# Optimization experiments

Hardware: AMD Instinct MI355X
Metric: run time of the kernel (lower is better)

## Reference

```python
import jax, jax.numpy as jnp
import numpy as np

N = 50000        # nodes
E = 800_000      # edges (avg degree 16)
D_IN, D_HID, D_OUT = 512, 512, 256
P_DROP = 0.5


def setup_inputs() -> dict:
    key = jax.random.key(0)
    k0, k1, k2, k3 = jax.random.split(key, 4)
    x = jax.random.normal(k0, (N, D_IN), dtype=jnp.float32)
    edge_index = jax.random.randint(k1, (2, E), 0, N, dtype=jnp.int64)
    W1 = jax.random.normal(k2, (D_HID, D_IN), dtype=jnp.float32) * 0.02
    b1 = jnp.zeros((D_HID,), dtype=jnp.float32)
    W2 = jax.random.normal(k3, (D_OUT, D_HID), dtype=jnp.float32) * 0.02
    b2 = jnp.zeros((D_OUT,), dtype=jnp.float32)
    return {"x": x, "edge_index": edge_index, "W1": W1, "b1": b1, "W2": W2, "b2": b2}


def _gcn_norm(edge_index, n):
    # add self loops, then symmetric GCN normalization: D^-1/2 (A+I) D^-1/2
    src, dst = edge_index[0], edge_index[1]
    loops = jnp.arange(n, dtype=src.dtype)
    src = jnp.concatenate([src, loops])
    dst = jnp.concatenate([dst, loops])
    deg = jax.ops.segment_sum(jnp.ones_like(src, dtype=jnp.float32), dst, num_segments=n)
    dinv = jax.lax.rsqrt(deg)  # deg >= 1 because of self loops
    norm = dinv[src] * dinv[dst]  # [E+N]
    return src, dst, norm


def _propagate(x, src, dst, norm):
    # out[i] = sum_{(j->i)} norm_e * x[j]
    return jax.ops.segment_sum(x[src] * norm[:, None], dst, num_segments=x.shape[0])


def reference(x, edge_index, W1, b1, W2, b2):
    src, dst, norm = _gcn_norm(edge_index, x.shape[0])
    # SGConv layer 1 (K=1): propagate then linear
    h = _propagate(x, src, dst, norm) @ W1.T + b1
    h = jax.nn.relu(h)
    # F.dropout(p) with training=True default -> deterministic fixed-key mask here
    keep = jax.random.bernoulli(jax.random.key(42), 1.0 - P_DROP, h.shape)
    embedding = jnp.where(keep, h / (1.0 - P_DROP), 0.0)
    # SGConv layer 2
    out = _propagate(embedding, src, dst, norm) @ W2.T + b2
    return embedding, out
```

## Files before the change

kernel.cpp:

```cpp
#include <hip/hip_runtime.h>

typedef unsigned short u16t;
typedef __attribute__((ext_vector_type(8))) short short8;
typedef __attribute__((ext_vector_type(4))) short short4v;
typedef __attribute__((ext_vector_type(4))) float f32x4;
typedef __attribute__((ext_vector_type(4))) unsigned short u16x4;

__device__ __forceinline__ float bf2f(short b) {
  return __uint_as_float(((unsigned)(unsigned short)b) << 16);
}
__device__ __forceinline__ u16t f2bf(float f) {
  unsigned u = __float_as_uint(f);
  u += 0x7FFFu + ((u >> 16) & 1u);
  return (u16t)(u >> 16);
}

__device__ __forceinline__ bool keep_mask(unsigned flat) {
  const unsigned k0 = 0u, k1 = 42u;
  const unsigned k2 = k0 ^ k1 ^ 0x1BD11BDAu;
  unsigned x0 = 0u + k0;
  unsigned x1 = flat + k1;
#define TF_R(r) { x0 += x1; x1 = (x1 << r) | (x1 >> (32 - r)); x1 ^= x0; }
  TF_R(13) TF_R(15) TF_R(26) TF_R(6)  x0 += k1; x1 += k2 + 1u;
  TF_R(17) TF_R(29) TF_R(16) TF_R(24) x0 += k2; x1 += k0 + 2u;
  TF_R(13) TF_R(15) TF_R(26) TF_R(6)  x0 += k0; x1 += k1 + 3u;
  TF_R(17) TF_R(29) TF_R(16) TF_R(24) x0 += k1; x1 += k2 + 4u;
  TF_R(13) TF_R(15) TF_R(26) TF_R(6)  x0 += k2; x1 += k0 + 5u;
#undef TF_R
  return ((x0 ^ x1) >> 31) == 0u;
}

__device__ __forceinline__ void load_lds16(const u16t* g, u16t* l) {
  __builtin_amdgcn_global_load_lds((__attribute__((address_space(1))) void*)g,
                                   (__attribute__((address_space(3))) void*)l,
                                   16, 0, 0);
}

__global__ void cvt_bf16(const float* __restrict__ s, u16t* __restrict__ d, int n) {
  int i = (blockIdx.x * 256 + threadIdx.x) * 4;
  if (i < n) {
    f32x4 v = *(const f32x4*)&s[i];
    u16x4 o = { f2bf(v.x), f2bf(v.y), f2bf(v.z), f2bf(v.w) };
    *(u16x4*)&d[i] = o;
  }
}

__global__ __launch_bounds__(256) void cvt_x_mask(const float* __restrict__ s,
    u16t* __restrict__ d, unsigned* __restrict__ mask, int n, int nwords) {
  int t = blockIdx.x * 256 + threadIdx.x;
  int i = t * 4;
  if (i < n) {
    f32x4 v = *(const f32x4*)&s[i];
    u16x4 o = { f2bf(v.x), f2bf(v.y), f2bf(v.z), f2bf(v.w) };
    *(u16x4*)&d[i] = o;
  }
  if (t < nwords) {
    unsigned base = (unsigned)t * 32u;
    unsigned m = 0u;
    for (int k = 0; k < 32; ++k) m |= (keep_mask(base + (unsigned)k) ? 1u : 0u) << k;
    mask[t] = m;
  }
}

__global__ void count_edges(const int* __restrict__ dst, int E, int* __restrict__ cnt) {
  int e = blockIdx.x * 256 + threadIdx.x;
  if (e < E) atomicAdd(&cnt[dst[e]], 1);
}

__global__ __launch_bounds__(256) void rowp_build(const int* __restrict__ cnt,
    int* __restrict__ rowp, int* __restrict__ cursor, float* __restrict__ dinv,
    int* __restrict__ gctr, int n) {
  __shared__ int sd[256];
  __shared__ int sbase;
  const int tid = threadIdx.x;
  const int i = blockIdx.x * 256 + tid;
  int c = (i < n) ? cnt[i] : 0;
  int v = c;
  sd[tid] = v;
  __syncthreads();
  for (int o = 1; o < 256; o <<= 1) {
    int t = (tid >= o) ? sd[tid - o] : 0;
    __syncthreads();
    v += t;
    sd[tid] = v;
    __syncthreads();
  }
  if (tid == 255) sbase = atomicAdd(gctr, v);
  __syncthreads();
  if (i < n) {
    int start = sbase + v - c;
    rowp[i] = start;
    cursor[i] = start;
    dinv[i] = rsqrtf((float)(c + 1));
  }
}

__global__ void fill_csr(const int* __restrict__ src, const int* __restrict__ dst, int E,
                         int* __restrict__ cursor, u16t* __restrict__ col) {
  int e = blockIdx.x * 256 + threadIdx.x;
  if (e < E) {
    int d = dst[e];
    int pos = atomicAdd(&cursor[d], 1);
    col[pos] = (u16t)src[e];
  }
}

__global__ __launch_bounds__(256) void gemm_bt_sl(const u16t* __restrict__ A,
                                                  const u16t* __restrict__ B,
                                                  u16t* __restrict__ C,
                                                  int K, int Mrows,
                                                  const float* __restrict__ dinv,
                                                  int Nclamp) {
  __shared__ __align__(16) u16t lA[128 * 32];
  __shared__ __align__(16) u16t lB[128 * 32];
  const int tid = threadIdx.x;
  const int wave = tid >> 6, lane = tid & 63;
  const int wm = (wave & 1) * 64, wn = (wave >> 1) * 64;
  const int lrow = lane & 15, lq = lane >> 4;
  const u16t* Ab = A + (size_t)blockIdx.x * 128 * K;
  const u16t* Bb = B + (size_t)blockIdx.y * 128 * K;
  const int r0 = tid >> 2, c0 = (tid & 3) * 8;
  const int ldsOff = __builtin_amdgcn_readfirstlane((tid >> 6) * 512);

  f32x4 acc[4][4];
  const f32x4 zero = {0.f, 0.f, 0.f, 0.f};
#pragma unroll
  for (int mi = 0; mi < 4; ++mi)
#pragma unroll
    for (int ni = 0; ni < 4; ++ni) acc[mi][ni] = zero;

  for (int kt = 0; kt < K; kt += 32) {
    __syncthreads();
    load_lds16(Ab + (size_t)r0 * K + kt + c0, &lA[ldsOff]);
    load_lds16(Ab + (size_t)(r0 + 64) * K + kt + c0, &lA[2048 + ldsOff]);
    load_lds16(Bb + (size_t)r0 * K + kt + c0, &lB[ldsOff]);
    load_lds16(Bb + (size_t)(r0 + 64) * K + kt + c0, &lB[2048 + ldsOff]);
    __syncthreads();
    short8 af[4], bfr[4];
#pragma unroll
    for (int mi = 0; mi < 4; ++mi)
      af[mi] = *(const short8*)&lA[(wm + mi * 16 + lrow) * 32 + lq * 8];
#pragma unroll
    for (int ni = 0; ni < 4; ++ni)
      bfr[ni] = *(const short8*)&lB[(wn + ni * 16 + lrow) * 32 + lq * 8];
#pragma unroll
    for (int mi = 0; mi < 4; ++mi)
#pragma unroll
      for (int ni = 0; ni < 4; ++ni)
        acc[mi][ni] = __builtin_amdgcn_mfma_f32_16x16x32_bf16(af[mi], bfr[ni], acc[mi][ni], 0, 0, 0);
  }

  const int crow0 = blockIdx.x * 128 + wm + lq * 4;
  const int ccol0 = blockIdx.y * 128 + wn + lrow;
#pragma unroll
  for (int mi = 0; mi < 4; ++mi)
#pragma unroll
    for (int r = 0; r < 4; ++r) {
      const int row = crow0 + mi * 16 + r;
      const float dr = dinv[row < Nclamp ? row : 0];
#pragma unroll
      for (int ni = 0; ni < 4; ++ni) {
        int cc = ccol0 + ni * 16;
        size_t idx = ((size_t)(cc >> 5) * Mrows + row) * 32 + (cc & 31);
        C[idx] = f2bf(dr * acc[mi][ni][r]);
      }
    }
}

__global__ __launch_bounds__(256) void prop1_kernel(const u16t* __restrict__ y1s,
    const u16t* __restrict__ colu, const int* __restrict__ rowp, const int* __restrict__ rowend,
    const float* __restrict__ dinv, const float* __restrict__ b1,
    const unsigned* __restrict__ kmask,
    float* __restrict__ embf, u16t* __restrict__ embb, int n, int Mrows, int chunks) {
  const int t = threadIdx.x;
  const int fl4 = (t & 7) * 4;
  const int bid = blockIdx.x;
  const int half = chunks << 3;
  const int phase = bid >= half;
  const int rem = bid - (phase ? half : 0);
  const int sl = (rem & 7) + (phase << 3);
  const int i = (rem >> 3) * 32 + (t >> 3);
  if (i >= n) return;

  const u16t* T = y1s + (size_t)sl * Mrows * 32 + fl4;
  const float di = dinv[i];
  float acc[4];
  {
    short4v u = *(const short4v*)&T[(size_t)i * 32];
#pragma unroll
    for (int j = 0; j < 4; ++j) acc[j] = bf2f(u[j]);
  }
  int e = rowp[i];
  const int e1 = rowend[i];
  if (e + 8 <= e1) {
    int c[8];
#pragma unroll
    for (int q = 0; q < 8; ++q) c[q] = (int)colu[e + q];
    e += 8;
    while (e + 8 <= e1) {
      int c2[8];
#pragma unroll
      for (int q = 0; q < 8; ++q) c2[q] = (int)colu[e + q];
#pragma unroll
      for (int q = 0; q < 8; ++q) {
        short4v u = *(const short4v*)&T[(size_t)c[q] * 32];
#pragma unroll
        for (int j = 0; j < 4; ++j) acc[j] += bf2f(u[j]);
      }
#pragma unroll
      for (int q = 0; q < 8; ++q) c[q] = c2[q];
      e += 8;
    }
#pragma unroll
    for (int q = 0; q < 8; ++q) {
      short4v u = *(const short4v*)&T[(size_t)c[q] * 32];
#pragma unroll
      for (int j = 0; j < 4; ++j) acc[j] += bf2f(u[j]);
    }
  }
  for (; e < e1; ++e) {
    short4v u = *(const short4v*)&T[(size_t)(int)colu[e] * 32];
#pragma unroll
    for (int j = 0; j < 4; ++j) acc[j] += bf2f(u[j]);
  }

  const int f = sl * 32 + fl4;
  const unsigned km = kmask[i * 16 + sl];
  f32x4 o;
  short4v ob;
#pragma unroll
  for (int j = 0; j < 4; ++j) {
    float h = di * acc[j] + b1[f + j];
    h = fmaxf(h, 0.f);
    float eb = ((km >> (fl4 + j)) & 1u) ? 2.f * h : 0.f;
    o[j] = eb;
    ob[j] = (short)f2bf(eb);
  }
  __builtin_nontemporal_store(o, (f32x4*)&embf[(size_t)i * 512 + f]);
  __builtin_nontemporal_store(ob, (short4v*)&embb[(size_t)i * 512 + f]);
}

__global__ __launch_bounds__(256) void prop2_kernel(const u16t* __restrict__ zs,
    const u16t* __restrict__ colu, const int* __restrict__ rowp, const int* __restrict__ rowend,
    const float* __restrict__ dinv, const float* __restrict__ b2,
    float* __restrict__ outp, int n, int Mrows, int chunks) {
  const int t = threadIdx.x;
  const int fl4 = (t & 7) * 4;
  const int bid = blockIdx.x;
  const int sl = bid & 7;
  const int i = (bid >> 3) * 32 + (t >> 3);
  (void)chunks;
  if (i >= n) return;

  const u16t* T = zs + (size_t)sl * Mrows * 32 + fl4;
  const float di = dinv[i];
  float acc[4];
  {
    short4v u = *(const short4v*)&T[(size_t)i * 32];
#pragma unroll
    for (int j = 0; j < 4; ++j) acc[j] = bf2f(u[j]);
  }
  int e = rowp[i];
  const int e1 = rowend[i];
  if (e + 8 <= e1) {
    int c[8];
#pragma unroll
    for (int q = 0; q < 8; ++q) c[q] = (int)colu[e + q];
    e += 8;
    while (e + 8 <= e1) {
      int c2[8];
#pragma unroll
      for (int q = 0; q < 8; ++q) c2[q] = (int)colu[e + q];
#pragma unroll
      for (int q = 0; q < 8; ++q) {
        short4v u = *(const short4v*)&T[(size_t)c[q] * 32];
#pragma unroll
        for (int j = 0; j < 4; ++j) acc[j] += bf2f(u[j]);
      }
#pragma unroll
      for (int q = 0; q < 8; ++q) c[q] = c2[q];
      e += 8;
    }
#pragma unroll
    for (int q = 0; q < 8; ++q) {
      short4v u = *(const short4v*)&T[(size_t)c[q] * 32];
#pragma unroll
      for (int j = 0; j < 4; ++j) acc[j] += bf2f(u[j]);
    }
  }
  for (; e < e1; ++e) {
    short4v u = *(const short4v*)&T[(size_t)(int)colu[e] * 32];
#pragma unroll
    for (int j = 0; j < 4; ++j) acc[j] += bf2f(u[j]);
  }

  const int f = sl * 32 + fl4;
  f32x4 o;
#pragma unroll
  for (int j = 0; j < 4; ++j) o[j] = di * acc[j] + b2[f + j];
  __builtin_nontemporal_store(o, (f32x4*)&outp[(size_t)i * 256 + f]);
}

extern "C" void kernel_launch(void* const* d_in, const int* in_sizes, int n_in,
                              void* d_out, int out_size, void* d_ws, size_t ws_size,
                              hipStream_t stream) {
  (void)n_in; (void)out_size; (void)ws_size;
  const float* x  = (const float*)d_in[0];
  const int*   ei = (const int*)d_in[1];
  const float* W1 = (const float*)d_in[2];
  const float* b1 = (const float*)d_in[3];
  const float* W2 = (const float*)d_in[4];
  const float* b2 = (const float*)d_in[5];

  const int Nn = in_sizes[0] / 512;
  const int E  = in_sizes[1] / 2;
  const int Mpad = ((Nn + 127) / 128) * 128;
  const int K = 512;
  const int CH = (Nn + 31) / 32;

  char* ws = (char*)d_ws;
  size_t off = 0;
  auto take = [&](size_t bytes) -> char* {
    char* p = ws + off;
    off += (bytes + 255) & ~(size_t)255;
    return p;
  };
  u16t* xb   = (u16t*)take((size_t)Mpad * 512 * 2);
  u16t* y1s  = (u16t*)take((size_t)16 * Mpad * 32 * 2);
  u16t* W1b  = (u16t*)take((size_t)512 * 512 * 2);
  u16t* W2b  = (u16t*)take((size_t)256 * 512 * 2);
  int*   cnt    = (int*)take((size_t)(Nn + 1) * 4);
  int*   rowp   = (int*)take((size_t)Nn * 4);
  int*   cursor = (int*)take((size_t)Nn * 4);
  float* dinv   = (float*)take((size_t)Nn * 4);
  u16t*  colu   = (u16t*)take((size_t)E * 2);
  unsigned* kmask = (unsigned*)take((size_t)Nn * 16 * 4);

  float* embf = (float*)d_out;
  float* outf = (float*)d_out + (size_t)Nn * 512;

  hipMemsetAsync(cnt, 0, (size_t)(Nn + 1) * 4, stream);

  const int n1 = Nn * 512;
  cvt_x_mask<<<(n1 / 4 + 255) / 256, 256, 0, stream>>>(x, xb, kmask, n1, Nn * 16);
  cvt_bf16<<<(512 * 512 / 4 + 255) / 256, 256, 0, stream>>>(W1, W1b, 512 * 512);
  cvt_bf16<<<(256 * 512 / 4 + 255) / 256, 256, 0, stream>>>(W2, W2b, 256 * 512);

  count_edges<<<(E + 255) / 256, 256, 0, stream>>>(ei + E, E, cnt);
  rowp_build<<<(Nn + 255) / 256, 256, 0, stream>>>(cnt, rowp, cursor, dinv, cnt + Nn, Nn);
  fill_csr<<<(E + 255) / 256, 256, 0, stream>>>(ei, ei + E, E, cursor, colu);

  dim3 g1(Mpad / 128, 4);
  gemm_bt_sl<<<g1, 256, 0, stream>>>(xb, W1b, y1s, K, Mpad, dinv, Nn);
  prop1_kernel<<<16 * CH, 256, 0, stream>>>(y1s, colu, rowp, cursor, dinv, b1, kmask,
                                            embf, xb , Nn, Mpad, CH);

  u16t* zs = y1s;
  dim3 g2(Mpad / 128, 2);
  gemm_bt_sl<<<g2, 256, 0, stream>>>(xb, W2b, zs, K, Mpad, dinv, Nn);
  prop2_kernel<<<8 * CH, 256, 0, stream>>>(zs, colu, rowp, cursor, dinv, b2, outf, Nn, Mpad, CH);
}
```

Measured before the change: 603.4 us.

## Pad CSR rows to multiples of eight and split gathers across thread pairs

The CSR build now folds the self-loop into the column list and pads each row to a multiple of eight entries. Padding points at a row that the GEMM epilogue now writes as zero. Row start, end and dinv are packed into one 16-byte descriptor per node. The propagation kernels assign two 8-lane groups per node, read eight column indices with one 16-byte load, gather without tail loops, and combine partial sums with a lane shuffle. This targets per-edge index-load latency and tail-loop divergence, at the cost of extra gathers of the padding row and more threads per node.

Result: slower. 623.9 us (+3.4%).

```diff
diff --git a/kernel.cpp b/kernel.cpp
--- a/kernel.cpp
+++ b/kernel.cpp
@@ -5,6 +5,8 @@
 typedef __attribute__((ext_vector_type(4))) short short4v;
 typedef __attribute__((ext_vector_type(4))) float f32x4;
 typedef __attribute__((ext_vector_type(4))) unsigned short u16x4;
+typedef __attribute__((ext_vector_type(4))) unsigned int u32x4;
+typedef __attribute__((ext_vector_type(4))) int i32x4;
 
 __device__ __forceinline__ float bf2f(short b) {
   return __uint_as_float(((unsigned)(unsigned short)b) << 16);
@@ -68,30 +70,37 @@
 }
 
 __global__ __launch_bounds__(256) void rowp_build(const int* __restrict__ cnt,
-    int* __restrict__ rowp, int* __restrict__ cursor, float* __restrict__ dinv,
-    int* __restrict__ gctr, int n) {
+    i32x4* __restrict__ ndr, int* __restrict__ cursor, float* __restrict__ dinv,
+    int* __restrict__ gctr, u16t* __restrict__ colu, int n) {
   __shared__ int sd[256];
   __shared__ int sbase;
   const int tid = threadIdx.x;
   const int i = blockIdx.x * 256 + tid;
   int c = (i < n) ? cnt[i] : 0;
-  int v = c;
+  int cs = c + 1;
+  int p = (i < n) ? ((cs + 7) & ~7) : 0;
+  int v = p;
   sd[tid] = v;
   __syncthreads();
   for (int o = 1; o < 256; o <<= 1) {
-    int t = (tid >= o) ? sd[tid - o] : 0;
+    int t2 = (tid >= o) ? sd[tid - o] : 0;
     __syncthreads();
-    v += t;
+    v += t2;
     sd[tid] = v;
     __syncthreads();
   }
   if (tid == 255) sbase = atomicAdd(gctr, v);
   __syncthreads();
   if (i < n) {
-    int start = sbase + v - c;
-    rowp[i] = start;
+    int start = sbase + v - p;
     cursor[i] = start;
-    dinv[i] = rsqrtf((float)(c + 1));
+    float dv = rsqrtf((float)cs);
+    dinv[i] = dv;
+    i32x4 r;
+    r[0] = start; r[1] = start + p; r[2] = __float_as_int(dv); r[3] = 0;
+    ndr[i] = r;
+    colu[start + c] = (u16t)i;
+    for (int q = c + 1; q < p; ++q) colu[start + q] = (u16t)n;
   }
 }
 
@@ -157,7 +166,7 @@
 #pragma unroll
     for (int r = 0; r < 4; ++r) {
       const int row = crow0 + mi * 16 + r;
-      const float dr = dinv[row < Nclamp ? row : 0];
+      const float dr = (row < Nclamp) ? dinv[row] : 0.f;
 #pragma unroll
       for (int ni = 0; ni < 4; ++ni) {
         int cc = ccol0 + ni * 16;
@@ -167,138 +176,118 @@
     }
 }
 
-__global__ __launch_bounds__(256) void prop1_kernel(const u16t* __restrict__ y1s,
-    const u16t* __restrict__ colu, const int* __restrict__ rowp, const int* __restrict__ rowend,
-    const float* __restrict__ dinv, const float* __restrict__ b1,
-    const unsigned* __restrict__ kmask,
+__device__ __forceinline__ void gather8(const u16t* __restrict__ T, u32x4 cw,
+                                        float acc[4]) {
+  int c[8];
+#pragma unroll
+  for (int q = 0; q < 4; ++q) {
+    c[2 * q]     = (int)(cw[q] & 0xFFFFu);
+    c[2 * q + 1] = (int)(cw[q] >> 16);
+  }
+  short4v u[8];
+#pragma unroll
+  for (int q = 0; q < 8; ++q) u[q] = *(const short4v*)&T[(size_t)c[q] * 32];
+#pragma unroll
+  for (int q = 0; q < 8; ++q)
+#pragma unroll
+    for (int j = 0; j < 4; ++j) acc[j] += bf2f(u[q][j]);
+}
+
+__global__ __launch_bounds__(256) void prop1_kernel(const u16t* __restrict__ T0,
+    const u16t* __restrict__ colu, const i32x4* __restrict__ ndr,
+    const float* __restrict__ b1, const unsigned* __restrict__ kmask,
     float* __restrict__ embf, u16t* __restrict__ embb, int n, int Mrows, int chunks) {
   const int t = threadIdx.x;
+  const int g = (t >> 3) & 1;
   const int fl4 = (t & 7) * 4;
   const int bid = blockIdx.x;
   const int half = chunks << 3;
   const int phase = bid >= half;
   const int rem = bid - (phase ? half : 0);
   const int sl = (rem & 7) + (phase << 3);
-  const int i = (rem >> 3) * 32 + (t >> 3);
+  const int i = (rem >> 3) * 16 + (t >> 4);
   if (i >= n) return;
 
-  const u16t* T = y1s + (size_t)sl * Mrows * 32 + fl4;
-  const float di = dinv[i];
-  float acc[4];
-  {
-    short4v u = *(const short4v*)&T[(size_t)i * 32];
-#pragma unroll
-    for (int j = 0; j < 4; ++j) acc[j] = bf2f(u[j]);
-  }
-  int e = rowp[i];
-  const int e1 = rowend[i];
-  if (e + 8 <= e1) {
-    int c[8];
-#pragma unroll
-    for (int q = 0; q < 8; ++q) c[q] = (int)colu[e + q];
-    e += 8;
-    while (e + 8 <= e1) {
-      int c2[8];
-#pragma unroll
-      for (int q = 0; q < 8; ++q) c2[q] = (int)colu[e + q];
-#pragma unroll
-      for (int q = 0; q < 8; ++q) {
-        short4v u = *(const short4v*)&T[(size_t)c[q] * 32];
-#pragma unroll
-        for (int j = 0; j < 4; ++j) acc[j] += bf2f(u[j]);
-      }
-#pragma unroll
-      for (int q = 0; q < 8; ++q) c[q] = c2[q];
-      e += 8;
+  const u16t* T = T0 + (size_t)sl * Mrows * 32 + fl4;
+  const i32x4 nd = ndr[i];
+  const float di = __int_as_float(nd[2]);
+  float acc[4] = {0.f, 0.f, 0.f, 0.f};
+
+  int e = nd[0] + g * 8;
+  const int end = nd[1];
+  if (e < end) {
+    u32x4 cw = *(const u32x4*)&colu[e];
+    e += 16;
+    while (e < end) {
+      u32x4 nw = *(const u32x4*)&colu[e];
+      e += 16;
+      gather8(T, cw, acc);
+      cw = nw;
     }
-#pragma unroll
-    for (int q = 0; q < 8; ++q) {
-      short4v u = *(const short4v*)&T[(size_t)c[q] * 32];
-#pragma unroll
-      for (int j = 0; j < 4; ++j) acc[j] += bf2f(u[j]);
+    gather8(T, cw, acc);
+  }
+
+#pragma unroll
+  for (int j = 0; j < 4; ++j) acc[j] += __shfl_xor(acc[j], 8, 64);
+
+  if ((t & 15) < 8) {
+    const int f = sl * 32 + fl4;
+    const unsigned km = kmask[i * 16 + sl];
+    f32x4 o;
+    short4v ob;
+#pragma unroll
+    for (int j = 0; j < 4; ++j) {
+      float h = di * acc[j] + b1[f + j];
+      h = fmaxf(h, 0.f);
+      float eb = ((km >> (fl4 + j)) & 1u) ? 2.f * h : 0.f;
+      o[j] = eb;
+      ob[j] = (short)f2bf(eb);
     }
-  }
-  for (; e < e1; ++e) {
-    short4v u = *(const short4v*)&T[(size_t)(int)colu[e] * 32];
-#pragma unroll
-    for (int j = 0; j < 4; ++j) acc[j] += bf2f(u[j]);
-  }
-
-  const int f = sl * 32 + fl4;
-  const unsigned km = kmask[i * 16 + sl];
-  f32x4 o;
-  short4v ob;
-#pragma unroll
-  for (int j = 0; j < 4; ++j) {
-    float h = di * acc[j] + b1[f + j];
-    h = fmaxf(h, 0.f);
-    float eb = ((km >> (fl4 + j)) & 1u) ? 2.f * h : 0.f;
-    o[j] = eb;
-    ob[j] = (short)f2bf(eb);
-  }
-  __builtin_nontemporal_store(o, (f32x4*)&embf[(size_t)i * 512 + f]);
-  __builtin_nontemporal_store(ob, (short4v*)&embb[(size_t)i * 512 + f]);
-}
-
-__global__ __launch_bounds__(256) void prop2_kernel(const u16t* __restrict__ zs,
-    const u16t* __restrict__ colu, const int* __restrict__ rowp, const int* __restrict__ rowend,
-    const float* __restrict__ dinv, const float* __restrict__ b2,
-    float* __restrict__ outp, int n, int Mrows, int chunks) {
+    __builtin_nontemporal_store(o, (f32x4*)&embf[(size_t)i * 512 + f]);
+    __builtin_nontemporal_store(ob, (short4v*)&embb[(size_t)i * 512 + f]);
+  }
+}
+
+__global__ __launch_bounds__(256) void prop2_kernel(const u16t* __restrict__ T0,
+    const u16t* __restrict__ colu, const i32x4* __restrict__ ndr,
+    const float* __restrict__ b2, float* __restrict__ outp, int n, int Mrows) {
   const int t = threadIdx.x;
+  const int g = (t >> 3) & 1;
   const int fl4 = (t & 7) * 4;
   const int bid = blockIdx.x;
   const int sl = bid & 7;
-  const int i = (bid >> 3) * 32 + (t >> 3);
-  (void)chunks;
+  const int i = (bid >> 3) * 16 + (t >> 4);
   if (i >= n) return;
 
-  const u16t* T = zs + (size_t)sl * Mrows * 32 + fl4;
-  const float di = dinv[i];
-  float acc[4];
-  {
-    short4v u = *(const short4v*)&T[(size_t)i * 32];
-#pragma unroll
-    for (int j = 0; j < 4; ++j) acc[j] = bf2f(u[j]);
-  }
-  int e = rowp[i];
-  const int e1 = rowend[i];
-  if (e + 8 <= e1) {
-    int c[8];
-#pragma unroll
-    for (int q = 0; q < 8; ++q) c[q] = (int)colu[e + q];
-    e += 8;
-    while (e + 8 <= e1) {
-      int c2[8];
-#pragma unroll
-      for (int q = 0; q < 8; ++q) c2[q] = (int)colu[e + q];
-#pragma unroll
-      for (int q = 0; q < 8; ++q) {
-        short4v u = *(const short4v*)&T[(size_t)c[q] * 32];
-#pragma unroll
-        for (int j = 0; j < 4; ++j) acc[j] += bf2f(u[j]);
-      }
-#pragma unroll
-      for (int q = 0; q < 8; ++q) c[q] = c2[q];
-      e += 8;
+  const u16t* T = T0 + (size_t)sl * Mrows * 32 + fl4;
+  const i32x4 nd = ndr[i];
+  const float di = __int_as_float(nd[2]);
+  float acc[4] = {0.f, 0.f, 0.f, 0.f};
+
+  int e = nd[0] + g * 8;
+  const int end = nd[1];
+  if (e < end) {
+    u32x4 cw = *(const u32x4*)&colu[e];
+    e += 16;
+    while (e < end) {
+      u32x4 nw = *(const u32x4*)&colu[e];
+      e += 16;
+      gather8(T, cw, acc);
+      cw = nw;
     }
-#pragma unroll
-    for (int q = 0; q < 8; ++q) {
-      short4v u = *(const short4v*)&T[(size_t)c[q] * 32];
-#pragma unroll
-      for (int j = 0; j < 4; ++j) acc[j] += bf2f(u[j]);
-    }
-  }
-  for (; e < e1; ++e) {
-    short4v u = *(const short4v*)&T[(size_t)(int)colu[e] * 32];
-#pragma unroll
-    for (int j = 0; j < 4; ++j) acc[j] += bf2f(u[j]);
-  }
-
-  const int f = sl * 32 + fl4;
-  f32x4 o;
-#pragma unroll
-  for (int j = 0; j < 4; ++j) o[j] = di * acc[j] + b2[f + j];
-  __builtin_nontemporal_store(o, (f32x4*)&outp[(size_t)i * 256 + f]);
+    gather8(T, cw, acc);
+  }
+
+#pragma unroll
+  for (int j = 0; j < 4; ++j) acc[j] += __shfl_xor(acc[j], 8, 64);
+
+  if ((t & 15) < 8) {
+    const int f = sl * 32 + fl4;
+    f32x4 o;
+#pragma unroll
+    for (int j = 0; j < 4; ++j) o[j] = di * acc[j] + b2[f + j];
+    __builtin_nontemporal_store(o, (f32x4*)&outp[(size_t)i * 256 + f]);
+  }
 }
 
 extern "C" void kernel_launch(void* const* d_in, const int* in_sizes, int n_in,
@@ -316,7 +305,7 @@
   const int E  = in_sizes[1] / 2;
   const int Mpad = ((Nn + 127) / 128) * 128;
   const int K = 512;
-  const int CH = (Nn + 31) / 32;
+  const int CH16 = (Nn + 15) / 16;
 
   char* ws = (char*)d_ws;
   size_t off = 0;
@@ -330,10 +319,10 @@
   u16t* W1b  = (u16t*)take((size_t)512 * 512 * 2);
   u16t* W2b  = (u16t*)take((size_t)256 * 512 * 2);
   int*   cnt    = (int*)take((size_t)(Nn + 1) * 4);
-  int*   rowp   = (int*)take((size_t)Nn * 4);
   int*   cursor = (int*)take((size_t)Nn * 4);
   float* dinv   = (float*)take((size_t)Nn * 4);
-  u16t*  colu   = (u16t*)take((size_t)E * 2);
+  i32x4* ndr    = (i32x4*)take((size_t)Nn * 16);
+  u16t*  colu   = (u16t*)take((size_t)(E + 8 * (Nn + 1)) * 2);
   unsigned* kmask = (unsigned*)take((size_t)Nn * 16 * 4);
 
   float* embf = (float*)d_out;
@@ -347,16 +336,17 @@
   cvt_bf16<<<(256 * 512 / 4 + 255) / 256, 256, 0, stream>>>(W2, W2b, 256 * 512);
 
   count_edges<<<(E + 255) / 256, 256, 0, stream>>>(ei + E, E, cnt);
-  rowp_build<<<(Nn + 255) / 256, 256, 0, stream>>>(cnt, rowp, cursor, dinv, cnt + Nn, Nn);
+  rowp_build<<<(Nn + 255) / 256, 256, 0, stream>>>(cnt, ndr, cursor, dinv, cnt + Nn,
+                                                   colu, Nn);
   fill_csr<<<(E + 255) / 256, 256, 0, stream>>>(ei, ei + E, E, cursor, colu);
 
   dim3 g1(Mpad / 128, 4);
   gemm_bt_sl<<<g1, 256, 0, stream>>>(xb, W1b, y1s, K, Mpad, dinv, Nn);
-  prop1_kernel<<<16 * CH, 256, 0, stream>>>(y1s, colu, rowp, cursor, dinv, b1, kmask,
-                                            embf, xb , Nn, Mpad, CH);
+  prop1_kernel<<<16 * CH16, 256, 0, stream>>>(y1s, colu, ndr, b1, kmask,
+                                              embf, xb , Nn, Mpad, CH16);
 
   u16t* zs = y1s;
   dim3 g2(Mpad / 128, 2);
   gemm_bt_sl<<<g2, 256, 0, stream>>>(xb, W2b, zs, K, Mpad, dinv, Nn);
-  prop2_kernel<<<8 * CH, 256, 0, stream>>>(zs, colu, rowp, cursor, dinv, b2, outf, Nn, Mpad, CH);
-}
+  prop2_kernel<<<8 * CH16, 256, 0, stream>>>(zs, colu, ndr, b2, outf, Nn, Mpad);
+}
```
